# Kernel optimization log

Hardware: AMD Instinct MI355X
Metric: run time of the kernel (lower is better)

## Reference

```python
import jax, jax.numpy as jnp
import numpy as np

NUM_Q = 1000
DIM_S = 64
SIZE_M = 50
BATCH = 128
SEQ = 200


def setup_inputs() -> dict:
    key = jax.random.key(0)
    ks = jax.random.split(key, 16)
    s = 1.0 / np.sqrt(DIM_S)
    inp = {
        "q": jax.random.randint(ks[0], (BATCH, SEQ), 0, NUM_Q),
        "r": jax.random.randint(ks[1], (BATCH, SEQ), 0, 2),
        "at_s": jax.random.randint(ks[2], (BATCH, 16), 0, 30000),
        "at_m": jnp.ones((BATCH, 16), dtype=jnp.int64 if jax.config.jax_enable_x64 else jnp.int32),
        "k_emb": jax.random.normal(ks[3], (NUM_Q, DIM_S)) * s,
        "v_emb": jax.random.normal(ks[4], (2 * NUM_Q, DIM_S)) * s,
        "Mk": jax.random.normal(ks[5], (SIZE_M, DIM_S)) * s,
        "Mv0": jax.random.normal(ks[6], (SIZE_M, DIM_S)) * s,
        "We": jax.random.normal(ks[7], (DIM_S, DIM_S)) * s,
        "be": jnp.zeros((DIM_S,)),
        "Wa": jax.random.normal(ks[8], (DIM_S, DIM_S)) * s,
        "ba": jnp.zeros((DIM_S,)),
        "Wf": jax.random.normal(ks[9], (2 * DIM_S, DIM_S)) * s,
        "bf": jnp.zeros((DIM_S,)),
        "Wp": jax.random.normal(ks[10], (DIM_S, 1)) * s,
        "bp": jnp.zeros((1,)),
    }
    return inp


def reference(q, r, at_s, at_m, k_emb, v_emb, Mk, Mv0, We, be, Wa, ba, Wf, bf, Wp, bp):
    num_q = k_emb.shape[0]
    x = q + r * num_q                         # [B, n]
    k = k_emb[q]                              # [B, n, d]
    v = v_emb[x]                              # [B, n, d]
    w = jax.nn.softmax(jnp.einsum("bnd,md->bnm", k, Mk), axis=-1)  # [B, n, m]
    e = jax.nn.sigmoid(v @ We + be)           # erase gate [B, n, d]
    a = jnp.tanh(v @ Wa + ba)                 # add vector [B, n, d]

    B = q.shape[0]
    Mv_init = jnp.broadcast_to(Mv0[None], (B,) + Mv0.shape)  # [B, m, d]

    def step(Mvt, inp):
        et, at_, wt = inp                     # [B,d], [B,d], [B,m]
        Mvt = Mvt * (1.0 - wt[:, :, None] * et[:, None, :]) + wt[:, :, None] * at_[:, None, :]
        return Mvt, Mvt

    xs = (e.transpose(1, 0, 2), a.transpose(1, 0, 2), w.transpose(1, 0, 2))
    _, Mv_seq = jax.lax.scan(step, Mv_init, xs)             # [n, B, m, d]
    Mv = jnp.concatenate([Mv_init[None], Mv_seq], axis=0)   # [n+1, B, m, d]
    Mv = Mv.transpose(1, 0, 2, 3)                            # [B, n+1, m, d]

    read = jnp.einsum("bnm,bnmd->bnd", w, Mv[:, :-1])        # read from pre-update memory
    f = jnp.tanh(jnp.concatenate([read, k], axis=-1) @ Wf + bf)
    p = jax.nn.sigmoid((f @ Wp + bp)).squeeze(-1)            # [B, n]; dropout is identity at eval
    return p, Mv
```

## Files before the change

### kernel.cpp

```cpp
#include <hip/hip_runtime.h>
#include <hip/hip_bf16.h>

typedef __hip_bfloat16 bf16;

#define BATCH 128
#define SEQ   200
#define NUMQ  1000
#define DD    64
#define MM    50
#define MH    25
#define CHUNKS 10
#define CLEN   20
#define RPB   16


__device__ __forceinline__ float rdlane(float v, int j) {
    return __uint_as_float(__builtin_amdgcn_readlane(__float_as_uint(v), j));
}

__global__ __launch_bounds__(256) void k1_wide(
    const int* __restrict__ q, const int* __restrict__ r,
    const float* __restrict__ k_emb, const float* __restrict__ v_emb,
    const float* __restrict__ Mk,
    const float* __restrict__ We, const float* __restrict__ be,
    const float* __restrict__ Wa, const float* __restrict__ ba,
    float* __restrict__ w_buf, float* __restrict__ e_buf, float* __restrict__ a_buf)
{
    __shared__ float Mk_l[MM][DD + 1];
    __shared__ float We_l[DD][DD + 1];
    __shared__ float Wa_l[DD][DD + 1];
    __shared__ float kv_l[4][128];

    const int tid  = threadIdx.x;
    const int w    = tid >> 6;
    const int lane = tid & 63;

    for (int i = tid; i < MM * DD; i += 256) Mk_l[i >> 6][i & 63] = Mk[i];
    for (int i = tid; i < DD * DD; i += 256) {
        We_l[i >> 6][i & 63] = We[i];
        Wa_l[i >> 6][i & 63] = Wa[i];
    }
    __syncthreads();

    const float be_l = be[lane];
    const float ba_l = ba[lane];
    const int row0 = blockIdx.x * RPB;

    for (int it = 0; it < RPB / 4; ++it) {
        const int row = row0 + it * 4 + w;

        int qi = q[row], ri = r[row];
        qi = min(max(qi, 0), NUMQ - 1);
        ri = min(max(ri, 0), 1);
        const int xi = qi + ri * NUMQ;

        kv_l[w][lane]      = k_emb[(size_t)qi * DD + lane];
        kv_l[w][64 + lane] = v_emb[(size_t)xi * DD + lane];

        float s = 0.f;
        if (lane < MM) {
            #pragma unroll
            for (int dd = 0; dd < DD; ++dd)
                s = __builtin_fmaf(kv_l[w][dd], Mk_l[lane][dd], s);
        }
        float mx = (lane < MM) ? s : -1e30f;
        #pragma unroll
        for (int off = 32; off >= 1; off >>= 1)
            mx = fmaxf(mx, __shfl_xor(mx, off, 64));
        float ex = (lane < MM) ? expf(s - mx) : 0.f;
        float sm = ex;
        #pragma unroll
        for (int off = 32; off >= 1; off >>= 1)
            sm += __shfl_xor(sm, off, 64);
        if (lane < MM)
            w_buf[(size_t)row * MM + lane] = ex / sm;

        float ea = be_l, aa = ba_l;
        #pragma unroll
        for (int dd = 0; dd < DD; ++dd) {
            const float vb = kv_l[w][64 + dd];
            ea = __builtin_fmaf(vb, We_l[dd][lane], ea);
            aa = __builtin_fmaf(vb, Wa_l[dd][lane], aa);
        }
        e_buf[(size_t)row * DD + lane] = 1.f / (1.f + expf(-ea));
        a_buf[(size_t)row * DD + lane] = tanhf(aa);
    }
}

__global__ __launch_bounds__(640) void k2_hier(
    const float* __restrict__ Mv0,
    const float* __restrict__ w_buf, const float* __restrict__ e_buf,
    const float* __restrict__ a_buf,
    float* __restrict__ read2_buf, float* __restrict__ out_Mv)
{
    __shared__ float POOL[CHUNKS * MH * DD];

    const int blk  = blockIdx.x;
    const int b    = blk >> 1;
    const int h    = blk & 1;
    const int tid  = threadIdx.x;
    const int wv   = tid >> 6;
    const int lane = tid & 63;
    const int t0   = wv * CLEN;
    const int mb   = h * MH;

    const float* wrow = w_buf + (size_t)b * SEQ * MM + mb;
    const float* erow = e_buf + (size_t)b * SEQ * DD;
    const float* arow = a_buf + (size_t)b * SEQ * DD;

    float A[MH], B[MH];
    #pragma unroll
    for (int j = 0; j < MH; ++j) { A[j] = 1.f; B[j] = 0.f; }

    float wreg = (lane < MH) ? wrow[(size_t)t0 * MM + lane] : 0.f;
    float e_n  = erow[(size_t)t0 * DD + lane];
    float a_n  = arow[(size_t)t0 * DD + lane];

    for (int tt = 0; tt < CLEN; ++tt) {
        const int t = t0 + tt;
        const float e_v = e_n, a_v = a_n, wcur = wreg;
        if (t + 1 < SEQ) {
            wreg = (lane < MH) ? wrow[(size_t)(t + 1) * MM + lane] : 0.f;
            e_n  = erow[(size_t)(t + 1) * DD + lane];
            a_n  = arow[(size_t)(t + 1) * DD + lane];
        }
        #pragma unroll
        for (int j = 0; j < MH; ++j) {
            const float wj = rdlane(wcur, j);
            const float f  = __builtin_fmaf(-wj, e_v, 1.f);
            A[j] *= f;
            B[j] = __builtin_fmaf(B[j], f, wj * a_v);
        }
    }

    float* outb = out_Mv + (size_t)b * (SEQ + 1) * MM * DD + (size_t)mb * DD;
    if (wv == 0) {
        #pragma unroll
        for (int j = 0; j < MH; ++j) {
            const float m0v = Mv0[(mb + j) * DD + lane];
            POOL[j * DD + lane] = m0v;
            outb[j * DD + lane] = m0v;
        }
    }
    __syncthreads();

    float Mv[MH];
    for (int w = 0; w < CHUNKS; ++w) {
        if (wv == w) {
            #pragma unroll
            for (int j = 0; j < MH; ++j) {
                Mv[j] = POOL[j * DD + lane];
                POOL[j * DD + lane] = __builtin_fmaf(A[j], Mv[j], B[j]);
            }
        }
        __syncthreads();
    }

    float* rrow = read2_buf + ((size_t)h * BATCH + b) * SEQ * DD;
    float* sp   = POOL + wv * (MH * DD);

    wreg = (lane < MH) ? wrow[(size_t)t0 * MM + lane] : 0.f;
    e_n  = erow[(size_t)t0 * DD + lane];
    a_n  = arow[(size_t)t0 * DD + lane];

    for (int tt = 0; tt < CLEN; ++tt) {
        const int t = t0 + tt;
        const float e_v = e_n, a_v = a_n, wcur = wreg;
        if (t + 1 < SEQ) {
            wreg = (lane < MH) ? wrow[(size_t)(t + 1) * MM + lane] : 0.f;
            e_n  = erow[(size_t)(t + 1) * DD + lane];
            a_n  = arow[(size_t)(t + 1) * DD + lane];
        }
        float racc0 = 0.f, racc1 = 0.f;
        #pragma unroll
        for (int j = 0; j < MH; ++j) {
            const float wj    = rdlane(wcur, j);
            const float m_old = Mv[j];
            if (j & 1) racc1 = __builtin_fmaf(wj, m_old, racc1);
            else       racc0 = __builtin_fmaf(wj, m_old, racc0);
            Mv[j] = __builtin_fmaf(wj, __builtin_fmaf(-e_v, m_old, a_v), m_old);
            sp[j * DD + lane] = Mv[j];
        }
        float* outt = outb + (size_t)(t + 1) * MM * DD;
        #pragma unroll
        for (int k = 0; k < 7; ++k) {
            const int f = lane + 64 * k;
            if (f < MH * DD / 4) {
                const float4 v4 = *reinterpret_cast<const float4*>(&sp[4 * f]);
                *reinterpret_cast<float4*>(&outt[4 * f]) = v4;
            }
        }
        rrow[(size_t)t * DD + lane] = racc0 + racc1;
    }
}

__global__ __launch_bounds__(256) void k3_wide(
    const int* __restrict__ q,
    const float* __restrict__ k_emb,
    const float* __restrict__ read2_buf,
    const float* __restrict__ Wf, const float* __restrict__ bfb,
    const float* __restrict__ Wp, const float* __restrict__ bp,
    float* __restrict__ out_p)
{
    __shared__ float Wf_l[2 * DD][DD + 1];
    __shared__ float rk[4][128];

    const int tid  = threadIdx.x;
    const int w    = tid >> 6;
    const int lane = tid & 63;

    for (int i = tid; i < 2 * DD * DD; i += 256)
        Wf_l[i >> 6][i & 63] = Wf[i];
    __syncthreads();

    const float bf_l = bfb[lane];
    const float wp_l = Wp[lane];
    const float bp0  = bp[0];
    const int row0 = blockIdx.x * RPB;

    const float* rd0 = read2_buf;
    const float* rd1 = read2_buf + (size_t)BATCH * SEQ * DD;

    for (int it = 0; it < RPB / 4; ++it) {
        const int row = row0 + it * 4 + w;

        int qi = q[row];
        qi = min(max(qi, 0), NUMQ - 1);
        rk[w][lane]      = rd0[(size_t)row * DD + lane] + rd1[(size_t)row * DD + lane];
        rk[w][64 + lane] = k_emb[(size_t)qi * DD + lane];

        float acc = bf_l;
        #pragma unroll
        for (int i = 0; i < 2 * DD; ++i)
            acc = __builtin_fmaf(rk[w][i], Wf_l[i][lane], acc);
        const float f = tanhf(acc);

        float pv = f * wp_l;
        #pragma unroll
        for (int off = 32; off >= 1; off >>= 1)
            pv += __shfl_xor(pv, off, 64);
        if (lane == 0)
            out_p[row] = 1.f / (1.f + expf(-(pv + bp0)));
    }
}

__global__ __launch_bounds__(640) void dkvmn_fused(
    const int* q_, const int* r_,
    const float* k_emb, const float* v_emb, const float* Mk, const float* Mv0,
    const float* We, const float* be, const float* Wa, const float* ba,
    const float* Wf, const float* bfb, const float* Wp, const float* bp,
    float* out_p, float* out_Mv)
{
    __shared__ float Mk_l[MM][DD + 1];
    __shared__ bf16  ring[SEQ][DD];
    __shared__ int   q_row[SEQ], x_row[SEQ];
    __shared__ float kbuf[DD], vbuf[DD], vbuf2[DD];
    __shared__ float wst[MM], est[DD], ast[DD];
    __shared__ float partial[640];
    __shared__ float bias_e[DD], bias_a[DD];

    const int b    = blockIdx.x;
    const int tid  = threadIdx.x;
    const int wv   = tid >> 6;
    const int lane = tid & 63;

    for (int t = tid; t < SEQ; t += 640) {
        int qi = q_[b * SEQ + t], ri = r_[b * SEQ + t];
        qi = min(max(qi, 0), NUMQ - 1); ri = min(max(ri, 0), 1);
        q_row[t] = qi; x_row[t] = qi + ri * NUMQ;
    }
    for (int i = tid; i < MM * DD; i += 640) Mk_l[i >> 6][i & 63] = Mk[i];
    if (tid < DD) { bias_e[tid] = be[tid]; bias_a[tid] = ba[tid]; }

    const int d  = lane;
    const int m0 = wv * 5;
    float* outb = out_Mv + (size_t)b * (SEQ + 1) * MM * DD;
    float Mv[5];
    #pragma unroll
    for (int j = 0; j < 5; ++j) {
        Mv[j] = Mv0[(m0 + j) * DD + d];
        outb[(m0 + j) * DD + d] = Mv[j];
    }
    __syncthreads();

    float kf_n = 0.f, vf_n = 0.f, vf2_n = 0.f;
    if (wv == 0) kf_n  = k_emb[(size_t)q_row[0] * DD + lane];
    if (wv == 1) vf_n  = v_emb[(size_t)x_row[0] * DD + lane];
    if (wv == 2) vf2_n = v_emb[(size_t)x_row[0] * DD + lane];

    for (int t = 0; t < SEQ; ++t) {
        if (wv == 0) {
            kbuf[lane] = kf_n;
            if (t + 1 < SEQ) kf_n = k_emb[(size_t)q_row[t + 1] * DD + lane];
            float s = 0.f;
            if (lane < MM) {
                #pragma unroll
                for (int dd = 0; dd < DD; ++dd) s += kbuf[dd] * Mk_l[lane][dd];
            }
            float mx = (lane < MM) ? s : -1e30f;
            #pragma unroll
            for (int off = 32; off >= 1; off >>= 1) mx = fmaxf(mx, __shfl_xor(mx, off, 64));
            float ex = (lane < MM) ? expf(s - mx) : 0.f;
            float sm = ex;
            #pragma unroll
            for (int off = 32; off >= 1; off >>= 1) sm += __shfl_xor(sm, off, 64);
            if (lane < MM) wst[lane] = ex / sm;
        } else if (wv == 1) {
            vbuf[lane] = vf_n;
            if (t + 1 < SEQ) vf_n = v_emb[(size_t)x_row[t + 1] * DD + lane];
            float acc = bias_e[lane];
            #pragma unroll
            for (int dd = 0; dd < DD; ++dd) acc += vbuf[dd] * We[dd * DD + lane];
            est[lane] = 1.f / (1.f + expf(-acc));
        } else if (wv == 2) {
            vbuf2[lane] = vf2_n;
            if (t + 1 < SEQ) vf2_n = v_emb[(size_t)x_row[t + 1] * DD + lane];
            float acc = bias_a[lane];
            #pragma unroll
            for (int dd = 0; dd < DD; ++dd) acc += vbuf2[dd] * Wa[dd * DD + lane];
            ast[lane] = tanhf(acc);
        }
        __syncthreads();

        const float e_v = est[d];
        const float a_v = ast[d];
        float racc = 0.f;
        float* outt = outb + (size_t)(t + 1) * MM * DD;
        #pragma unroll
        for (int j = 0; j < 5; ++j) {
            const float wvv = wst[m0 + j];
            racc += wvv * Mv[j];
            Mv[j] = __builtin_fmaf(wvv, a_v - e_v * Mv[j], Mv[j]);
            outt[(m0 + j) * DD + d] = Mv[j];
        }
        partial[tid] = racc;
        __syncthreads();

        if (tid < DD) {
            float rr = 0.f;
            #pragma unroll
            for (int g = 0; g < 10; ++g) rr += partial[g * 64 + tid];
            ring[t][tid] = (bf16)rr;
        }
    }
    __syncthreads();

    for (int t = wv; t < SEQ; t += 10) {
        const int qi = q_row[t];
        const float kreg = k_emb[(size_t)qi * DD + lane];
        float acc = bfb[lane];
        #pragma unroll
        for (int i = 0; i < DD; ++i) acc += (float)ring[t][i] * Wf[i * DD + lane];
        #pragma unroll
        for (int i = 0; i < DD; ++i) acc += __shfl(kreg, i, 64) * Wf[(DD + i) * DD + lane];
        const float f = tanhf(acc);
        float pv = f * Wp[lane];
        #pragma unroll
        for (int off = 32; off >= 1; off >>= 1) pv += __shfl_xor(pv, off, 64);
        if (lane == 0)
            out_p[(size_t)b * SEQ + t] = 1.f / (1.f + expf(-(pv + bp[0])));
    }
}

extern "C" void kernel_launch(void* const* d_in, const int* in_sizes, int n_in,
                              void* d_out, int out_size, void* d_ws, size_t ws_size,
                              hipStream_t stream) {
    const int*   q     = (const int*)  d_in[0];
    const int*   r     = (const int*)  d_in[1];
    const float* k_emb = (const float*)d_in[4];
    const float* v_emb = (const float*)d_in[5];
    const float* Mk    = (const float*)d_in[6];
    const float* Mv0   = (const float*)d_in[7];
    const float* We    = (const float*)d_in[8];
    const float* be    = (const float*)d_in[9];
    const float* Wa    = (const float*)d_in[10];
    const float* ba    = (const float*)d_in[11];
    const float* Wf    = (const float*)d_in[12];
    const float* bfb   = (const float*)d_in[13];
    const float* Wp    = (const float*)d_in[14];
    const float* bp    = (const float*)d_in[15];

    float* out_p  = (float*)d_out;
    float* out_Mv = (float*)d_out + BATCH * SEQ;

    const size_t N_W  = (size_t)BATCH * SEQ * MM;
    const size_t N_D  = (size_t)BATCH * SEQ * DD;
    const size_t WS_NEEDED = (N_W + 4 * N_D) * sizeof(float);

    const int rows = BATCH * SEQ;

    if (ws_size >= WS_NEEDED) {
        float* w_buf     = (float*)d_ws;
        float* e_buf     = w_buf + N_W;
        float* a_buf     = e_buf + N_D;
        float* read2_buf = a_buf + N_D;

        hipLaunchKernelGGL(k1_wide, dim3(rows / RPB), dim3(256), 0, stream,
                           q, r, k_emb, v_emb, Mk, We, be, Wa, ba, w_buf, e_buf, a_buf);
        hipLaunchKernelGGL(k2_hier, dim3(BATCH * 2), dim3(640), 0, stream,
                           Mv0, w_buf, e_buf, a_buf, read2_buf, out_Mv);
        hipLaunchKernelGGL(k3_wide, dim3(rows / RPB), dim3(256), 0, stream,
                           q, k_emb, read2_buf, Wf, bfb, Wp, bp, out_p);
    } else {
        hipLaunchKernelGGL(dkvmn_fused, dim3(BATCH), dim3(640), 0, stream,
                           q, r, k_emb, v_emb, Mk, Mv0, We, be, Wa, ba,
                           Wf, bfb, Wp, bp, out_p, out_Mv);
    }
}
```

Baseline: 153.5 us.

## Fuse embedding/gate projection kernel into the scan kernel and batch read stores

Removes the separate k1 kernel and computes softmax weights, erase and add gates inside the scan kernel, interleaved with the chunk-local A/B accumulation pass. The point is to save a kernel launch and to overlap the gate projections with the scan work. In exchange, each of the two half-memory blocks per batch recomputes the full projections, and private per-half e/a buffers are written to the workspace and read back. Read outputs are also staged in shared memory and written as float4 every four steps, which adds shared-memory use (now over 100KB per block) and may limit occupancy.

```diff
diff --git a/kernel.cpp b/kernel.cpp
--- a/kernel.cpp
+++ b/kernel.cpp
@@ -18,82 +18,20 @@
     return __uint_as_float(__builtin_amdgcn_readlane(__float_as_uint(v), j));
 }
 
-__global__ __launch_bounds__(256) void k1_wide(
-    const int* __restrict__ q, const int* __restrict__ r,
+__global__ __launch_bounds__(640) void k2_mega(
+    const int* __restrict__ q_, const int* __restrict__ r_,
     const float* __restrict__ k_emb, const float* __restrict__ v_emb,
-    const float* __restrict__ Mk,
+    const float* __restrict__ Mk, const float* __restrict__ Mv0,
     const float* __restrict__ We, const float* __restrict__ be,
     const float* __restrict__ Wa, const float* __restrict__ ba,
-    float* __restrict__ w_buf, float* __restrict__ e_buf, float* __restrict__ a_buf)
+    float* __restrict__ w_buf, float* __restrict__ e2_buf, float* __restrict__ a2_buf,
+    float* __restrict__ read2_buf, float* __restrict__ out_Mv)
 {
     __shared__ float Mk_l[MM][DD + 1];
-    __shared__ float We_l[DD][DD + 1];
-    __shared__ float Wa_l[DD][DD + 1];
-    __shared__ float kv_l[4][128];
-
-    const int tid  = threadIdx.x;
-    const int w    = tid >> 6;
-    const int lane = tid & 63;
-
-    for (int i = tid; i < MM * DD; i += 256) Mk_l[i >> 6][i & 63] = Mk[i];
-    for (int i = tid; i < DD * DD; i += 256) {
-        We_l[i >> 6][i & 63] = We[i];
-        Wa_l[i >> 6][i & 63] = Wa[i];
-    }
-    __syncthreads();
-
-    const float be_l = be[lane];
-    const float ba_l = ba[lane];
-    const int row0 = blockIdx.x * RPB;
-
-    for (int it = 0; it < RPB / 4; ++it) {
-        const int row = row0 + it * 4 + w;
-
-        int qi = q[row], ri = r[row];
-        qi = min(max(qi, 0), NUMQ - 1);
-        ri = min(max(ri, 0), 1);
-        const int xi = qi + ri * NUMQ;
-
-        kv_l[w][lane]      = k_emb[(size_t)qi * DD + lane];
-        kv_l[w][64 + lane] = v_emb[(size_t)xi * DD + lane];
-
-        float s = 0.f;
-        if (lane < MM) {
-            #pragma unroll
-            for (int dd = 0; dd < DD; ++dd)
-                s = __builtin_fmaf(kv_l[w][dd], Mk_l[lane][dd], s);
-        }
-        float mx = (lane < MM) ? s : -1e30f;
-        #pragma unroll
-        for (int off = 32; off >= 1; off >>= 1)
-            mx = fmaxf(mx, __shfl_xor(mx, off, 64));
-        float ex = (lane < MM) ? expf(s - mx) : 0.f;
-        float sm = ex;
-        #pragma unroll
-        for (int off = 32; off >= 1; off >>= 1)
-            sm += __shfl_xor(sm, off, 64);
-        if (lane < MM)
-            w_buf[(size_t)row * MM + lane] = ex / sm;
-
-        float ea = be_l, aa = ba_l;
-        #pragma unroll
-        for (int dd = 0; dd < DD; ++dd) {
-            const float vb = kv_l[w][64 + dd];
-            ea = __builtin_fmaf(vb, We_l[dd][lane], ea);
-            aa = __builtin_fmaf(vb, Wa_l[dd][lane], aa);
-        }
-        e_buf[(size_t)row * DD + lane] = 1.f / (1.f + expf(-ea));
-        a_buf[(size_t)row * DD + lane] = tanhf(aa);
-    }
-}
-
-__global__ __launch_bounds__(640) void k2_hier(
-    const float* __restrict__ Mv0,
-    const float* __restrict__ w_buf, const float* __restrict__ e_buf,
-    const float* __restrict__ a_buf,
-    float* __restrict__ read2_buf, float* __restrict__ out_Mv)
-{
+    __shared__ float We_l[DD][DD];
+    __shared__ float Wa_l[DD][DD];
     __shared__ float POOL[CHUNKS * MH * DD];
+    __shared__ float RBUF[CHUNKS][4 * DD];
 
     const int blk  = blockIdx.x;
     const int b    = blk >> 1;
@@ -104,72 +42,121 @@
     const int t0   = wv * CLEN;
     const int mb   = h * MH;
 
-    const float* wrow = w_buf + (size_t)b * SEQ * MM + mb;
-    const float* erow = e_buf + (size_t)b * SEQ * DD;
-    const float* arow = a_buf + (size_t)b * SEQ * DD;
+    for (int i = tid; i < MM * DD; i += 640) Mk_l[i >> 6][i & 63] = Mk[i];
+    for (int i = tid; i < DD * DD; i += 640) {
+        We_l[i >> 6][i & 63] = We[i];
+        Wa_l[i >> 6][i & 63] = Wa[i];
+    }
+    const float be_l = be[lane];
+    const float ba_l = ba[lane];
+    __syncthreads();
+
+    float* kv = RBUF[wv];
 
     float A[MH], B[MH];
     #pragma unroll
     for (int j = 0; j < MH; ++j) { A[j] = 1.f; B[j] = 0.f; }
 
+    int qi = min(max(q_[b * SEQ + t0], 0), NUMQ - 1);
+    int ri = min(max(r_[b * SEQ + t0], 0), 1);
+    float kf = k_emb[(size_t)qi * DD + lane];
+    float vf = v_emb[(size_t)(qi + ri * NUMQ) * DD + lane];
+
+    float* e2row = e2_buf + (size_t)(h * BATCH + b) * SEQ * DD;
+    float* a2row = a2_buf + (size_t)(h * BATCH + b) * SEQ * DD;
+
+    for (int tt = 0; tt < CLEN; ++tt) {
+        const int t   = t0 + tt;
+        const int row = b * SEQ + t;
+        const float kcur = kf, vcur = vf;
+        if (t + 1 < SEQ) {
+            int qn = min(max(q_[row + 1], 0), NUMQ - 1);
+            int rn = min(max(r_[row + 1], 0), 1);
+            kf = k_emb[(size_t)qn * DD + lane];
+            vf = v_emb[(size_t)(qn + rn * NUMQ) * DD + lane];
+        }
+        kv[lane]      = kcur;
+        kv[64 + lane] = vcur;
+
+        float s = 0.f;
+        if (lane < MM) {
+            #pragma unroll
+            for (int dd = 0; dd < DD; ++dd)
+                s = __builtin_fmaf(kv[dd], Mk_l[lane][dd], s);
+        }
+        float mx = (lane < MM) ? s : -1e30f;
+        #pragma unroll
+        for (int off = 32; off >= 1; off >>= 1)
+            mx = fmaxf(mx, __shfl_xor(mx, off, 64));
+        float ex = (lane < MM) ? expf(s - mx) : 0.f;
+        float sm = ex;
+        #pragma unroll
+        for (int off = 32; off >= 1; off >>= 1)
+            sm += __shfl_xor(sm, off, 64);
+        const float wm = ex / sm;
+        if (lane >= mb && lane < mb + MH)
+            w_buf[(size_t)row * MM + lane] = wm;
+
+        float ea = be_l, aa = ba_l;
+        #pragma unroll
+        for (int dd = 0; dd < DD; ++dd) {
+            const float vb = kv[64 + dd];
+            ea = __builtin_fmaf(vb, We_l[dd][lane], ea);
+            aa = __builtin_fmaf(vb, Wa_l[dd][lane], aa);
+        }
+        const float e_v = 1.f / (1.f + expf(-ea));
+        const float a_v = tanhf(aa);
+        e2row[(size_t)t * DD + lane] = e_v;
+        a2row[(size_t)t * DD + lane] = a_v;
+
+        #pragma unroll
+        for (int j = 0; j < MH; ++j) {
+            const float wj = rdlane(wm, mb + j);
+            const float f  = __builtin_fmaf(-wj, e_v, 1.f);
+            A[j] *= f;
+            B[j] = __builtin_fmaf(B[j], f, wj * a_v);
+        }
+    }
+
+    float* outb = out_Mv + (size_t)b * (SEQ + 1) * MM * DD + (size_t)mb * DD;
+    if (wv == 0) {
+        #pragma unroll
+        for (int j = 0; j < MH; ++j) {
+            const float m0v = Mv0[(mb + j) * DD + lane];
+            POOL[j * DD + lane] = m0v;
+            outb[j * DD + lane] = m0v;
+        }
+    }
+    __syncthreads();
+
+    float Mv[MH];
+    for (int w = 0; w < CHUNKS; ++w) {
+        if (wv == w) {
+            #pragma unroll
+            for (int j = 0; j < MH; ++j) {
+                Mv[j] = POOL[j * DD + lane];
+                POOL[j * DD + lane] = __builtin_fmaf(A[j], Mv[j], B[j]);
+            }
+        }
+        __syncthreads();
+    }
+
+    const float* wrow = w_buf + (size_t)b * SEQ * MM + mb;
+    float* rrow = read2_buf + (size_t)(h * BATCH + b) * SEQ * DD;
+    float* sp   = POOL + wv * (MH * DD);
+    float* rb   = RBUF[wv];
+
     float wreg = (lane < MH) ? wrow[(size_t)t0 * MM + lane] : 0.f;
-    float e_n  = erow[(size_t)t0 * DD + lane];
-    float a_n  = arow[(size_t)t0 * DD + lane];
+    float e_n  = e2row[(size_t)t0 * DD + lane];
+    float a_n  = a2row[(size_t)t0 * DD + lane];
 
     for (int tt = 0; tt < CLEN; ++tt) {
         const int t = t0 + tt;
         const float e_v = e_n, a_v = a_n, wcur = wreg;
         if (t + 1 < SEQ) {
             wreg = (lane < MH) ? wrow[(size_t)(t + 1) * MM + lane] : 0.f;
-            e_n  = erow[(size_t)(t + 1) * DD + lane];
-            a_n  = arow[(size_t)(t + 1) * DD + lane];
-        }
-        #pragma unroll
-        for (int j = 0; j < MH; ++j) {
-            const float wj = rdlane(wcur, j);
-            const float f  = __builtin_fmaf(-wj, e_v, 1.f);
-            A[j] *= f;
-            B[j] = __builtin_fmaf(B[j], f, wj * a_v);
-        }
-    }
-
-    float* outb = out_Mv + (size_t)b * (SEQ + 1) * MM * DD + (size_t)mb * DD;
-    if (wv == 0) {
-        #pragma unroll
-        for (int j = 0; j < MH; ++j) {
-            const float m0v = Mv0[(mb + j) * DD + lane];
-            POOL[j * DD + lane] = m0v;
-            outb[j * DD + lane] = m0v;
-        }
-    }
-    __syncthreads();
-
-    float Mv[MH];
-    for (int w = 0; w < CHUNKS; ++w) {
-        if (wv == w) {
-            #pragma unroll
-            for (int j = 0; j < MH; ++j) {
-                Mv[j] = POOL[j * DD + lane];
-                POOL[j * DD + lane] = __builtin_fmaf(A[j], Mv[j], B[j]);
-            }
-        }
-        __syncthreads();
-    }
-
-    float* rrow = read2_buf + ((size_t)h * BATCH + b) * SEQ * DD;
-    float* sp   = POOL + wv * (MH * DD);
-
-    wreg = (lane < MH) ? wrow[(size_t)t0 * MM + lane] : 0.f;
-    e_n  = erow[(size_t)t0 * DD + lane];
-    a_n  = arow[(size_t)t0 * DD + lane];
-
-    for (int tt = 0; tt < CLEN; ++tt) {
-        const int t = t0 + tt;
-        const float e_v = e_n, a_v = a_n, wcur = wreg;
-        if (t + 1 < SEQ) {
-            wreg = (lane < MH) ? wrow[(size_t)(t + 1) * MM + lane] : 0.f;
-            e_n  = erow[(size_t)(t + 1) * DD + lane];
-            a_n  = arow[(size_t)(t + 1) * DD + lane];
+            e_n  = e2row[(size_t)(t + 1) * DD + lane];
+            a_n  = a2row[(size_t)(t + 1) * DD + lane];
         }
         float racc0 = 0.f, racc1 = 0.f;
         #pragma unroll
@@ -190,7 +177,11 @@
                 *reinterpret_cast<float4*>(&outt[4 * f]) = v4;
             }
         }
-        rrow[(size_t)t * DD + lane] = racc0 + racc1;
+        rb[(tt & 3) * DD + lane] = racc0 + racc1;
+        if ((tt & 3) == 3) {
+            const float4 v4 = *reinterpret_cast<const float4*>(&rb[4 * lane]);
+            *reinterpret_cast<float4*>(&rrow[(size_t)(t0 + tt - 3) * DD + 4 * lane]) = v4;
+        }
     }
 }
 
@@ -385,20 +376,19 @@
 
     const size_t N_W  = (size_t)BATCH * SEQ * MM;
     const size_t N_D  = (size_t)BATCH * SEQ * DD;
-    const size_t WS_NEEDED = (N_W + 4 * N_D) * sizeof(float);
+    const size_t WS_NEEDED = (N_W + 6 * N_D) * sizeof(float);
 
     const int rows = BATCH * SEQ;
 
     if (ws_size >= WS_NEEDED) {
         float* w_buf     = (float*)d_ws;
-        float* e_buf     = w_buf + N_W;
-        float* a_buf     = e_buf + N_D;
-        float* read2_buf = a_buf + N_D;
-
-        hipLaunchKernelGGL(k1_wide, dim3(rows / RPB), dim3(256), 0, stream,
-                           q, r, k_emb, v_emb, Mk, We, be, Wa, ba, w_buf, e_buf, a_buf);
-        hipLaunchKernelGGL(k2_hier, dim3(BATCH * 2), dim3(640), 0, stream,
-                           Mv0, w_buf, e_buf, a_buf, read2_buf, out_Mv);
+        float* e2_buf    = w_buf + N_W;
+        float* a2_buf    = e2_buf + 2 * N_D;
+        float* read2_buf = a2_buf + 2 * N_D;
+
+        hipLaunchKernelGGL(k2_mega, dim3(BATCH * 2), dim3(640), 0, stream,
+                           q, r, k_emb, v_emb, Mk, Mv0, We, be, Wa, ba,
+                           w_buf, e2_buf, a2_buf, read2_buf, out_Mv);
         hipLaunchKernelGGL(k3_wide, dim3(rows / RPB), dim3(256), 0, stream,
                            q, k_emb, read2_buf, Wf, bfb, Wp, bp, out_p);
     } else {
```

Result: slower. 286.0 us (+86.3%).

## Fuse three-stage pipeline into one cooperative kernel with grid syncs

Applied to the files above, without the earlier changes.

Replaces the three separate launches (gate precompute, chunked scan, output projection) with a single cooperative kernel of 256 blocks that runs the three phases separated by grid.sync(), keeping weights in shared memory across phases. The aim is to remove the launch gaps and tail effects between kernels. The Mv output writes are staged through shared memory and stored as float4. The old per-batch fused fallback is removed, so the path taken when workspace is too small now does nothing, and grid syncs add their own barrier cost.

```diff
diff --git a/kernel.cpp b/kernel.cpp
--- a/kernel.cpp
+++ b/kernel.cpp
@@ -1,6 +1,8 @@
 #include <hip/hip_runtime.h>
+#include <hip/hip_cooperative_groups.h>
 #include <hip/hip_bf16.h>
 
+namespace cg = cooperative_groups;
 typedef __hip_bfloat16 bf16;
 
 #define BATCH 128
@@ -16,6 +18,221 @@
 
 __device__ __forceinline__ float rdlane(float v, int j) {
     return __uint_as_float(__builtin_amdgcn_readlane(__float_as_uint(v), j));
+}
+
+__global__ __launch_bounds__(640) void dkvmn_coop(
+    const int* __restrict__ q_, const int* __restrict__ r_,
+    const float* __restrict__ k_emb, const float* __restrict__ v_emb,
+    const float* __restrict__ Mk, const float* __restrict__ Mv0,
+    const float* __restrict__ We, const float* __restrict__ be,
+    const float* __restrict__ Wa, const float* __restrict__ ba,
+    const float* __restrict__ Wf, const float* __restrict__ bfb,
+    const float* __restrict__ Wp, const float* __restrict__ bp,
+    float* __restrict__ w_buf, float* __restrict__ e_buf, float* __restrict__ a_buf,
+    float* __restrict__ read2_buf, float* __restrict__ out_p, float* __restrict__ out_Mv)
+{
+    __shared__ float POOL[24320];
+    __shared__ float RBUF[CHUNKS][256];
+
+    cg::grid_group grid = cg::this_grid();
+
+    const int tid  = threadIdx.x;
+    const int wv   = tid >> 6;
+    const int lane = tid & 63;
+
+    float* Mk_l = POOL;
+    float* We_l = POOL + 3250;
+    float* Wa_l = POOL + 7346;
+    float* Wf_l = POOL + 16000;
+
+    for (int i = tid; i < MM * DD; i += 640) Mk_l[(i >> 6) * 65 + (i & 63)] = Mk[i];
+    for (int i = tid; i < DD * DD; i += 640) { We_l[i] = We[i]; Wa_l[i] = Wa[i]; }
+    for (int i = tid; i < 2 * DD * DD; i += 640) Wf_l[(i >> 6) * 65 + (i & 63)] = Wf[i];
+    const float be_l = be[lane];
+    const float ba_l = ba[lane];
+    __syncthreads();
+
+    {
+        const int gw   = blockIdx.x * CHUNKS + wv;
+        const int row0 = gw * 10;
+        float* kv = RBUF[wv];
+
+        int qi = min(max(q_[row0], 0), NUMQ - 1);
+        int ri = min(max(r_[row0], 0), 1);
+        float kf = k_emb[(size_t)qi * DD + lane];
+        float vf = v_emb[(size_t)(qi + ri * NUMQ) * DD + lane];
+
+        for (int i = 0; i < 10; ++i) {
+            const int rr = row0 + i;
+            const float kcur = kf, vcur = vf;
+            if (i + 1 < 10) {
+                int qn = min(max(q_[rr + 1], 0), NUMQ - 1);
+                int rn = min(max(r_[rr + 1], 0), 1);
+                kf = k_emb[(size_t)qn * DD + lane];
+                vf = v_emb[(size_t)(qn + rn * NUMQ) * DD + lane];
+            }
+            kv[lane]      = kcur;
+            kv[64 + lane] = vcur;
+
+            float s = 0.f;
+            if (lane < MM) {
+                #pragma unroll
+                for (int dd = 0; dd < DD; ++dd)
+                    s = __builtin_fmaf(kv[dd], Mk_l[lane * 65 + dd], s);
+            }
+            float mx = (lane < MM) ? s : -1e30f;
+            #pragma unroll
+            for (int off = 32; off >= 1; off >>= 1)
+                mx = fmaxf(mx, __shfl_xor(mx, off, 64));
+            float ex = (lane < MM) ? expf(s - mx) : 0.f;
+            float sm = ex;
+            #pragma unroll
+            for (int off = 32; off >= 1; off >>= 1)
+                sm += __shfl_xor(sm, off, 64);
+            if (lane < MM)
+                w_buf[(size_t)rr * MM + lane] = ex / sm;
+
+            float ea = be_l, aa = ba_l;
+            #pragma unroll
+            for (int dd = 0; dd < DD; ++dd) {
+                const float vb = kv[64 + dd];
+                ea = __builtin_fmaf(vb, We_l[dd * DD + lane], ea);
+                aa = __builtin_fmaf(vb, Wa_l[dd * DD + lane], aa);
+            }
+            e_buf[(size_t)rr * DD + lane] = 1.f / (1.f + expf(-ea));
+            a_buf[(size_t)rr * DD + lane] = tanhf(aa);
+        }
+    }
+    grid.sync();
+
+    {
+        const int blk = blockIdx.x;
+        const int b   = blk >> 1;
+        const int h   = blk & 1;
+        const int t0  = wv * CLEN;
+        const int mb  = h * MH;
+
+        const float* wrow = w_buf + (size_t)b * SEQ * MM + mb;
+        const float* erow = e_buf + (size_t)b * SEQ * DD;
+        const float* arow = a_buf + (size_t)b * SEQ * DD;
+
+        float A[MH], B[MH];
+        #pragma unroll
+        for (int j = 0; j < MH; ++j) { A[j] = 1.f; B[j] = 0.f; }
+
+        float wreg = (lane < MH) ? wrow[(size_t)t0 * MM + lane] : 0.f;
+        float e_n  = erow[(size_t)t0 * DD + lane];
+        float a_n  = arow[(size_t)t0 * DD + lane];
+
+        for (int tt = 0; tt < CLEN; ++tt) {
+            const int t = t0 + tt;
+            const float e_v = e_n, a_v = a_n, wcur = wreg;
+            if (t + 1 < SEQ) {
+                wreg = (lane < MH) ? wrow[(size_t)(t + 1) * MM + lane] : 0.f;
+                e_n  = erow[(size_t)(t + 1) * DD + lane];
+                a_n  = arow[(size_t)(t + 1) * DD + lane];
+            }
+            #pragma unroll
+            for (int j = 0; j < MH; ++j) {
+                const float wj = rdlane(wcur, j);
+                const float f  = __builtin_fmaf(-wj, e_v, 1.f);
+                A[j] *= f;
+                B[j] = __builtin_fmaf(B[j], f, wj * a_v);
+            }
+        }
+
+        float* outb = out_Mv + (size_t)b * (SEQ + 1) * MM * DD + (size_t)mb * DD;
+        if (wv == 0) {
+            #pragma unroll
+            for (int j = 0; j < MH; ++j) {
+                const float m0v = Mv0[(mb + j) * DD + lane];
+                POOL[j * DD + lane] = m0v;
+                outb[j * DD + lane] = m0v;
+            }
+        }
+        __syncthreads();
+
+        float Mv[MH];
+        for (int w = 0; w < CHUNKS; ++w) {
+            if (wv == w) {
+                #pragma unroll
+                for (int j = 0; j < MH; ++j) {
+                    Mv[j] = POOL[j * DD + lane];
+                    POOL[j * DD + lane] = __builtin_fmaf(A[j], Mv[j], B[j]);
+                }
+            }
+            __syncthreads();
+        }
+
+        float* rrow = read2_buf + (size_t)(h * BATCH + b) * SEQ * DD;
+        float* sp   = POOL + wv * (MH * DD);
+
+        wreg = (lane < MH) ? wrow[(size_t)t0 * MM + lane] : 0.f;
+        e_n  = erow[(size_t)t0 * DD + lane];
+        a_n  = arow[(size_t)t0 * DD + lane];
+
+        for (int tt = 0; tt < CLEN; ++tt) {
+            const int t = t0 + tt;
+            const float e_v = e_n, a_v = a_n, wcur = wreg;
+            if (t + 1 < SEQ) {
+                wreg = (lane < MH) ? wrow[(size_t)(t + 1) * MM + lane] : 0.f;
+                e_n  = erow[(size_t)(t + 1) * DD + lane];
+                a_n  = arow[(size_t)(t + 1) * DD + lane];
+            }
+            float racc0 = 0.f, racc1 = 0.f;
+            #pragma unroll
+            for (int j = 0; j < MH; ++j) {
+                const float wj    = rdlane(wcur, j);
+                const float m_old = Mv[j];
+                if (j & 1) racc1 = __builtin_fmaf(wj, m_old, racc1);
+                else       racc0 = __builtin_fmaf(wj, m_old, racc0);
+                Mv[j] = __builtin_fmaf(wj, __builtin_fmaf(-e_v, m_old, a_v), m_old);
+                sp[j * DD + lane] = Mv[j];
+            }
+            float* outt = outb + (size_t)(t + 1) * MM * DD;
+            #pragma unroll
+            for (int k = 0; k < 7; ++k) {
+                const int f = lane + 64 * k;
+                if (f < MH * DD / 4) {
+                    const float4 v4 = *reinterpret_cast<const float4*>(&sp[4 * f]);
+                    *reinterpret_cast<float4*>(&outt[4 * f]) = v4;
+                }
+            }
+            rrow[(size_t)t * DD + lane] = racc0 + racc1;
+        }
+    }
+    grid.sync();
+
+    {
+        const int gw   = blockIdx.x * CHUNKS + wv;
+        const int row0 = gw * 10;
+        float* rk = RBUF[wv];
+        const float bf_l = bfb[lane];
+        const float wp_l = Wp[lane];
+        const float bp0  = bp[0];
+        const float* rd0 = read2_buf;
+        const float* rd1 = read2_buf + (size_t)BATCH * SEQ * DD;
+
+        for (int i = 0; i < 10; ++i) {
+            const int rr = row0 + i;
+            int qi = min(max(q_[rr], 0), NUMQ - 1);
+            rk[lane]      = rd0[(size_t)rr * DD + lane] + rd1[(size_t)rr * DD + lane];
+            rk[64 + lane] = k_emb[(size_t)qi * DD + lane];
+
+            float acc = bf_l;
+            #pragma unroll
+            for (int ii = 0; ii < 2 * DD; ++ii)
+                acc = __builtin_fmaf(rk[ii], Wf_l[ii * 65 + lane], acc);
+            const float f = tanhf(acc);
+
+            float pv = f * wp_l;
+            #pragma unroll
+            for (int off = 32; off >= 1; off >>= 1)
+                pv += __shfl_xor(pv, off, 64);
+            if (lane == 0)
+                out_p[rr] = 1.f / (1.f + expf(-(pv + bp0)));
+        }
+    }
 }
 
 __global__ __launch_bounds__(256) void k1_wide(
@@ -48,7 +265,6 @@
 
     for (int it = 0; it < RPB / 4; ++it) {
         const int row = row0 + it * 4 + w;
-
         int qi = q[row], ri = r[row];
         qi = min(max(qi, 0), NUMQ - 1);
         ri = min(max(ri, 0), 1);
@@ -223,7 +439,6 @@
 
     for (int it = 0; it < RPB / 4; ++it) {
         const int row = row0 + it * 4 + w;
-
         int qi = q[row];
         qi = min(max(qi, 0), NUMQ - 1);
         rk[w][lane]      = rd0[(size_t)row * DD + lane] + rd1[(size_t)row * DD + lane];
@@ -241,124 +456,6 @@
             pv += __shfl_xor(pv, off, 64);
         if (lane == 0)
             out_p[row] = 1.f / (1.f + expf(-(pv + bp0)));
-    }
-}
-
-__global__ __launch_bounds__(640) void dkvmn_fused(
-    const int* q_, const int* r_,
-    const float* k_emb, const float* v_emb, const float* Mk, const float* Mv0,
-    const float* We, const float* be, const float* Wa, const float* ba,
-    const float* Wf, const float* bfb, const float* Wp, const float* bp,
-    float* out_p, float* out_Mv)
-{
-    __shared__ float Mk_l[MM][DD + 1];
-    __shared__ bf16  ring[SEQ][DD];
-    __shared__ int   q_row[SEQ], x_row[SEQ];
-    __shared__ float kbuf[DD], vbuf[DD], vbuf2[DD];
-    __shared__ float wst[MM], est[DD], ast[DD];
-    __shared__ float partial[640];
-    __shared__ float bias_e[DD], bias_a[DD];
-
-    const int b    = blockIdx.x;
-    const int tid  = threadIdx.x;
-    const int wv   = tid >> 6;
-    const int lane = tid & 63;
-
-    for (int t = tid; t < SEQ; t += 640) {
-        int qi = q_[b * SEQ + t], ri = r_[b * SEQ + t];
-        qi = min(max(qi, 0), NUMQ - 1); ri = min(max(ri, 0), 1);
-        q_row[t] = qi; x_row[t] = qi + ri * NUMQ;
-    }
-    for (int i = tid; i < MM * DD; i += 640) Mk_l[i >> 6][i & 63] = Mk[i];
-    if (tid < DD) { bias_e[tid] = be[tid]; bias_a[tid] = ba[tid]; }
-
-    const int d  = lane;
-    const int m0 = wv * 5;
-    float* outb = out_Mv + (size_t)b * (SEQ + 1) * MM * DD;
-    float Mv[5];
-    #pragma unroll
-    for (int j = 0; j < 5; ++j) {
-        Mv[j] = Mv0[(m0 + j) * DD + d];
-        outb[(m0 + j) * DD + d] = Mv[j];
-    }
-    __syncthreads();
-
-    float kf_n = 0.f, vf_n = 0.f, vf2_n = 0.f;
-    if (wv == 0) kf_n  = k_emb[(size_t)q_row[0] * DD + lane];
-    if (wv == 1) vf_n  = v_emb[(size_t)x_row[0] * DD + lane];
-    if (wv == 2) vf2_n = v_emb[(size_t)x_row[0] * DD + lane];
-
-    for (int t = 0; t < SEQ; ++t) {
-        if (wv == 0) {
-            kbuf[lane] = kf_n;
-            if (t + 1 < SEQ) kf_n = k_emb[(size_t)q_row[t + 1] * DD + lane];
-            float s = 0.f;
-            if (lane < MM) {
-                #pragma unroll
-                for (int dd = 0; dd < DD; ++dd) s += kbuf[dd] * Mk_l[lane][dd];
-            }
-            float mx = (lane < MM) ? s : -1e30f;
-            #pragma unroll
-            for (int off = 32; off >= 1; off >>= 1) mx = fmaxf(mx, __shfl_xor(mx, off, 64));
-            float ex = (lane < MM) ? expf(s - mx) : 0.f;
-            float sm = ex;
-            #pragma unroll
-            for (int off = 32; off >= 1; off >>= 1) sm += __shfl_xor(sm, off, 64);
-            if (lane < MM) wst[lane] = ex / sm;
-        } else if (wv == 1) {
-            vbuf[lane] = vf_n;
-            if (t + 1 < SEQ) vf_n = v_emb[(size_t)x_row[t + 1] * DD + lane];
-            float acc = bias_e[lane];
-            #pragma unroll
-            for (int dd = 0; dd < DD; ++dd) acc += vbuf[dd] * We[dd * DD + lane];
-            est[lane] = 1.f / (1.f + expf(-acc));
-        } else if (wv == 2) {
-            vbuf2[lane] = vf2_n;
-            if (t + 1 < SEQ) vf2_n = v_emb[(size_t)x_row[t + 1] * DD + lane];
-            float acc = bias_a[lane];
-            #pragma unroll
-            for (int dd = 0; dd < DD; ++dd) acc += vbuf2[dd] * Wa[dd * DD + lane];
-            ast[lane] = tanhf(acc);
-        }
-        __syncthreads();
-
-        const float e_v = est[d];
-        const float a_v = ast[d];
-        float racc = 0.f;
-        float* outt = outb + (size_t)(t + 1) * MM * DD;
-        #pragma unroll
-        for (int j = 0; j < 5; ++j) {
-            const float wvv = wst[m0 + j];
-            racc += wvv * Mv[j];
-            Mv[j] = __builtin_fmaf(wvv, a_v - e_v * Mv[j], Mv[j]);
-            outt[(m0 + j) * DD + d] = Mv[j];
-        }
-        partial[tid] = racc;
-        __syncthreads();
-
-        if (tid < DD) {
-            float rr = 0.f;
-            #pragma unroll
-            for (int g = 0; g < 10; ++g) rr += partial[g * 64 + tid];
-            ring[t][tid] = (bf16)rr;
-        }
-    }
-    __syncthreads();
-
-    for (int t = wv; t < SEQ; t += 10) {
-        const int qi = q_row[t];
-        const float kreg = k_emb[(size_t)qi * DD + lane];
-        float acc = bfb[lane];
-        #pragma unroll
-        for (int i = 0; i < DD; ++i) acc += (float)ring[t][i] * Wf[i * DD + lane];
-        #pragma unroll
-        for (int i = 0; i < DD; ++i) acc += __shfl(kreg, i, 64) * Wf[(DD + i) * DD + lane];
-        const float f = tanhf(acc);
-        float pv = f * Wp[lane];
-        #pragma unroll
-        for (int off = 32; off >= 1; off >>= 1) pv += __shfl_xor(pv, off, 64);
-        if (lane == 0)
-            out_p[(size_t)b * SEQ + t] = 1.f / (1.f + expf(-(pv + bp[0])));
     }
 }
 
@@ -395,15 +492,35 @@
         float* a_buf     = e_buf + N_D;
         float* read2_buf = a_buf + N_D;
 
-        hipLaunchKernelGGL(k1_wide, dim3(rows / RPB), dim3(256), 0, stream,
-                           q, r, k_emb, v_emb, Mk, We, be, Wa, ba, w_buf, e_buf, a_buf);
-        hipLaunchKernelGGL(k2_hier, dim3(BATCH * 2), dim3(640), 0, stream,
-                           Mv0, w_buf, e_buf, a_buf, read2_buf, out_Mv);
-        hipLaunchKernelGGL(k3_wide, dim3(rows / RPB), dim3(256), 0, stream,
-                           q, k_emb, read2_buf, Wf, bfb, Wp, bp, out_p);
+        int dev = 0;
+        hipGetDevice(&dev);
+        hipDeviceProp_t props;
+        hipError_t perr = hipGetDeviceProperties(&props, dev);
+        bool try_coop = (perr == hipSuccess) && (props.cooperativeLaunch != 0);
+
+        hipError_t lerr = hipErrorUnknown;
+        if (try_coop) {
+            void* args[] = {
+                (void*)&q, (void*)&r, (void*)&k_emb, (void*)&v_emb,
+                (void*)&Mk, (void*)&Mv0, (void*)&We, (void*)&be,
+                (void*)&Wa, (void*)&ba, (void*)&Wf, (void*)&bfb,
+                (void*)&Wp, (void*)&bp,
+                (void*)&w_buf, (void*)&e_buf, (void*)&a_buf, (void*)&read2_buf,
+                (void*)&out_p, (void*)&out_Mv
+            };
+            lerr = hipLaunchCooperativeKernel((const void*)dkvmn_coop,
+                                              dim3(BATCH * 2), dim3(640),
+                                              args, 0, stream);
+        }
+        if (lerr != hipSuccess) {
+            hipLaunchKernelGGL(k1_wide, dim3(rows / RPB), dim3(256), 0, stream,
+                               q, r, k_emb, v_emb, Mk, We, be, Wa, ba,
+                               w_buf, e_buf, a_buf);
+            hipLaunchKernelGGL(k2_hier, dim3(BATCH * 2), dim3(640), 0, stream,
+                               Mv0, w_buf, e_buf, a_buf, read2_buf, out_Mv);
+            hipLaunchKernelGGL(k3_wide, dim3(rows / RPB), dim3(256), 0, stream,
+                               q, k_emb, read2_buf, Wf, bfb, Wp, bp, out_p);
+        }
     } else {
-        hipLaunchKernelGGL(dkvmn_fused, dim3(BATCH), dim3(640), 0, stream,
-                           q, r, k_emb, v_emb, Mk, Mv0, We, be, Wa, ba,
-                           Wf, bfb, Wp, bp, out_p, out_Mv);
     }
 }
```

Result: slower. 216.3 us (+40.9%).
